# Performance work log

Hardware: AMD Instinct MI355X
Metric: run time of the kernel (lower is better)

## Reference

```python
import jax, jax.numpy as jnp
import numpy as np
from jax import lax

SCALE = 2
K_UP = 5
EPS = 1e-5
DN = ('NCHW', 'OIHW', 'NCHW')


def _bn(x, gamma, beta, mean, var):
    inv = gamma / jnp.sqrt(var + EPS)
    return x * inv[None, :, None, None] + (beta - mean * inv)[None, :, None, None]


def _pixel_shuffle(x, r):
    b, crr, h, w = x.shape
    c = crr // (r * r)
    x = x.reshape(b, c, r, r, h, w)
    x = x.transpose(0, 1, 4, 2, 5, 3)  # b, c, h, r, w, r
    return x.reshape(b, c, h * r, w * r)


def setup_inputs() -> dict:
    key = jax.random.key(0)
    ks = jax.random.split(key, 4)
    b, c, h, w = 4, 64, 128, 128
    c_mid = 64
    enc_out = (SCALE * K_UP) ** 2  # 100
    return {
        'X': jax.random.normal(ks[0], (b, c, h, w), jnp.float32),
        'comp_w': jax.random.normal(ks[1], (c_mid, c, 1, 1), jnp.float32) * 0.1,
        'comp_gamma': jnp.ones((c_mid,), jnp.float32),
        'comp_beta': jnp.zeros((c_mid,), jnp.float32),
        'comp_mean': jnp.zeros((c_mid,), jnp.float32),
        'comp_var': jnp.ones((c_mid,), jnp.float32),
        'enc_w': jax.random.normal(ks[2], (enc_out, c_mid, 3, 3), jnp.float32) * 0.05,
        'enc_b': jnp.zeros((enc_out,), jnp.float32),
        'enc_gamma': jnp.ones((enc_out,), jnp.float32),
        'enc_beta': jnp.zeros((enc_out,), jnp.float32),
        'enc_mean': jnp.zeros((enc_out,), jnp.float32),
        'enc_var': jnp.ones((enc_out,), jnp.float32),
    }


def reference(X, comp_w, comp_gamma, comp_beta, comp_mean, comp_var,
              enc_w, enc_b, enc_gamma, enc_beta, enc_mean, enc_var):
    b, c, h, w = X.shape
    h_, w_ = h * SCALE, w * SCALE
    # compress: 1x1 conv + BN + ReLU
    Wm = lax.conv_general_dilated(X, comp_w, (1, 1), 'VALID', dimension_numbers=DN)
    Wm = jax.nn.relu(_bn(Wm, comp_gamma, comp_beta, comp_mean, comp_var))
    # encode kernel weights: 3x3 conv + BN
    Wm = lax.conv_general_dilated(Wm, enc_w, (1, 1), ((1, 1), (1, 1)), dimension_numbers=DN)
    Wm = Wm + enc_b[None, :, None, None]
    Wm = _bn(Wm, enc_gamma, enc_beta, enc_mean, enc_var)
    # pixel shuffle -> [b, k_up^2, h_, w_], softmax over kernel dim
    Wm = _pixel_shuffle(Wm, SCALE)
    Wm = jax.nn.softmax(Wm, axis=1)
    # nearest upsample input
    Xu = jnp.repeat(jnp.repeat(X, SCALE, axis=2), SCALE, axis=3)  # [b,c,h_,w_]
    # unfold(k=5, dilation=2, pad=4) + einsum, fused as accumulation over the
    # 25 kernel taps (avoids the b*c*25*h_*w_ im2col blowup; identical math)
    pad = (K_UP // 2) * SCALE  # 4
    Xp = jnp.pad(Xu, ((0, 0), (0, 0), (pad, pad), (pad, pad)))
    out = jnp.zeros((b, c, h_, w_), X.dtype)
    for i in range(K_UP):
        for j in range(K_UP):
            k = i * K_UP + j
            patch = lax.dynamic_slice(Xp, (0, 0, i * SCALE, j * SCALE), (b, c, h_, w_))
            out = out + Wm[:, k:k + 1] * patch
    return out
```

## Files before the change

### kernel.cpp

```cpp
#include <hip/hip_runtime.h>

#define EPS 1e-5f

typedef __attribute__((ext_vector_type(8))) short short8;
typedef __attribute__((ext_vector_type(4))) float float4v;

__device__ inline unsigned short f2bf(float f) {
  unsigned u = __float_as_uint(f);
  unsigned r = (u + 0x7fffu + ((u >> 16) & 1u)) >> 16;
  return (unsigned short)r;
}
__device__ inline uint pk2(float a, float b) {
  return (uint)f2bf(a) | ((uint)f2bf(b) << 16);
}

__global__ __launch_bounds__(256) void xform_kernel(
    const float* __restrict__ enc_w, const float* __restrict__ enc_gamma,
    const float* __restrict__ enc_var, const float* __restrict__ comp_w,
    const float* __restrict__ comp_gamma, const float* __restrict__ comp_var,
    ushort* __restrict__ Awt, float* __restrict__ Wc) {
  int u = blockIdx.x * 256 + threadIdx.x;
  if (u < 9216) {
    int kc = u >> 9, rem = u & 511;
    int mt = rem >> 6, q = (rem >> 4) & 3, ml = rem & 15;
    int e = mt * 16 + ml;
    int t = kc >> 1, h = kc & 1;
    int dy = t / 3, dx = t - dy * 3;
    float inv = (e < 100) ? enc_gamma[e] * rsqrtf(enc_var[e] + EPS) : 0.f;
    ushort o[8];
#pragma unroll
    for (int j = 0; j < 8; ++j) {
      int ci = h * 32 + q * 8 + j;
      float w = (e < 100) ? enc_w[(e * 64 + ci) * 9 + dy * 3 + dx] * inv : 0.f;
      o[j] = f2bf(w);
    }
    uint4 v;
    v.x = (uint)o[0] | ((uint)o[1] << 16);
    v.y = (uint)o[2] | ((uint)o[3] << 16);
    v.z = (uint)o[4] | ((uint)o[5] << 16);
    v.w = (uint)o[6] | ((uint)o[7] << 16);
    *reinterpret_cast<uint4*>(Awt + (size_t)u * 8) = v;
  } else if (u < 9216 + 4096) {
    int v = u - 9216;
    int co = v & 63;
    float inv = comp_gamma[co] * rsqrtf(comp_var[co] + EPS);
    Wc[v] = comp_w[co * 64 + (v >> 6)] * inv;
  }
}

__global__ void bias_kernel(
    const float* __restrict__ enc_b, const float* __restrict__ enc_gamma,
    const float* __restrict__ enc_beta, const float* __restrict__ enc_mean,
    const float* __restrict__ enc_var, const float* __restrict__ comp_gamma,
    const float* __restrict__ comp_beta, const float* __restrict__ comp_mean,
    const float* __restrict__ comp_var, float* __restrict__ bias2,
    float* __restrict__ bias_c) {
  int t = threadIdx.x;
  if (t < 128) {
    float v = 0.f;
    if (t < 100) {
      float inv = enc_gamma[t] * rsqrtf(enc_var[t] + EPS);
      v = enc_b[t] * inv + enc_beta[t] - enc_mean[t] * inv;
    }
    bias2[t] = v;
  } else if (t < 192) {
    int c = t - 128;
    float inv = comp_gamma[c] * rsqrtf(comp_var[c] + EPS);
    bias_c[c] = comp_beta[c] - comp_mean[c] * inv;
  }
}

__global__ __launch_bounds__(256) void compress_kernel(
    const float* __restrict__ X, const float* __restrict__ Wc,
    const float* __restrict__ bias_c, ushort* __restrict__ out,
    ushort* __restrict__ Xb) {
  __shared__ __align__(16) float xtile[64 * 65];
  __shared__ __align__(16) float osm[64 * 68];
  const int tid = threadIdx.x;
  const int p0 = blockIdx.x * 64;
  const int b = p0 >> 14;
  const float* xbase = X + ((size_t)b << 20) + (p0 & 16383);

#pragma unroll
  for (int k = 0; k < 16; ++k) {
    int u = k * 256 + tid;
    int ci = u >> 6, px = u & 63;
    xtile[px * 65 + ci] = xbase[((size_t)ci << 14) + px];
  }
  __syncthreads();

  const int wv = __builtin_amdgcn_readfirstlane(tid >> 6);
  const int ln = tid & 63;
  float acc[16];
#pragma unroll
  for (int u = 0; u < 16; ++u) acc[u] = bias_c[wv * 16 + u];
  const float* xr = xtile + ln * 65;
#pragma unroll 8
  for (int ci = 0; ci < 64; ++ci) {
    float xv = xr[ci];
    const float* wr = Wc + ci * 64 + wv * 16;
#pragma unroll
    for (int u = 0; u < 16; ++u) acc[u] = fmaf(wr[u], xv, acc[u]);
  }
  float4v* orow = reinterpret_cast<float4v*>(osm) + ln * 17 + wv * 4;
#pragma unroll
  for (int j = 0; j < 4; ++j) {
    float4v t;
#pragma unroll
    for (int s = 0; s < 4; ++s) t[s] = fmaxf(acc[j * 4 + s], 0.f);
    orow[j] = t;
  }
  __syncthreads();

#pragma unroll
  for (int j = 0; j < 2; ++j) {
    int u = j * 256 + tid;
    int px = u >> 3, g = u & 7;
    const float* so = osm + px * 68 + g * 8;
    uint4 vo = make_uint4(pk2(so[0], so[1]), pk2(so[2], so[3]),
                          pk2(so[4], so[5]), pk2(so[6], so[7]));
    *reinterpret_cast<uint4*>(out + (size_t)(p0 + px) * 64 + g * 8) = vo;
    const float* sx = xtile + px * 65 + g * 8;
    uint4 vx = make_uint4(pk2(sx[0], sx[1]), pk2(sx[2], sx[3]),
                          pk2(sx[4], sx[5]), pk2(sx[6], sx[7]));
    *reinterpret_cast<uint4*>(Xb + (size_t)(p0 + px) * 64 + g * 8) = vx;
  }
}

__global__ __launch_bounds__(256) void encode_mfma(
    const ushort* __restrict__ Wm1t, const ushort* __restrict__ Awt,
    const float* __restrict__ bias2, uint* __restrict__ Wtu) {
  __shared__ __align__(16) char smem[25600];
  ushort* Xt = (ushort*)smem;
  const int tid = threadIdx.x;
  const int b = blockIdx.z;
  const int y0 = blockIdx.y * 8, x0 = blockIdx.x * 8;

  for (int u = tid; u < 800; u += 256) {
    int pos = u >> 3, cg = u & 7;
    int iy = pos / 10, ix = pos - iy * 10;
    int gy = y0 + iy - 1, gx = x0 + ix - 1;
    uint4 v = make_uint4(0, 0, 0, 0);
    if ((unsigned)gy < 128u && (unsigned)gx < 128u)
      v = *reinterpret_cast<const uint4*>(
          Wm1t + ((((size_t)b << 14) + (gy << 7) + gx) << 6) + cg * 8);
    *reinterpret_cast<uint4*>(&Xt[pos * 72 + cg * 8]) = v;
  }
  __syncthreads();

  const int wave = tid >> 6, lane = tid & 63;
  const int q = lane >> 4, px16 = lane & 15;

  float4v acc[2][4];
#pragma unroll
  for (int a = 0; a < 2; ++a)
#pragma unroll
    for (int n = 0; n < 4; ++n) acc[a][n] = (float4v){0.f, 0.f, 0.f, 0.f};

  const short8* Ap = reinterpret_cast<const short8*>(Awt);
#pragma unroll
  for (int kc = 0; kc < 18; ++kc) {
    const int t = kc >> 1, h = kc & 1;
    const int dy = t / 3, dx = t - dy * 3;
    short8 af[2];
#pragma unroll
    for (int a = 0; a < 2; ++a)
      af[a] = Ap[kc * 512 + (wave * 2 + a) * 64 + lane];
    short8 bfr[4];
#pragma unroll
    for (int n = 0; n < 4; ++n) {
      int p = n * 16 + px16;
      int iy = (p >> 3) + dy, ix = (p & 7) + dx;
      bfr[n] = *reinterpret_cast<const short8*>(
          &Xt[(iy * 10 + ix) * 72 + h * 32 + q * 8]);
    }
#pragma unroll
    for (int a = 0; a < 2; ++a)
#pragma unroll
      for (int n = 0; n < 4; ++n)
        acc[a][n] = __builtin_amdgcn_mfma_f32_16x16x32_bf16(
            af[a], bfr[n], acc[a][n], 0, 0, 0);
  }
  __syncthreads();

  float* wsm = (float*)smem;
#pragma unroll
  for (int a = 0; a < 2; ++a) {
    int ebase = (wave * 2 + a) * 16 + q * 4;
    if (ebase < 100) {
#pragma unroll
      for (int n = 0; n < 4; ++n) {
        int p = n * 16 + px16;
        *reinterpret_cast<float4v*>(wsm + p * 100 + ebase) = acc[a][n];
      }
    }
  }
  __syncthreads();

  if (tid < 64) {
    const float4v* bias4 = (const float4v*)bias2;
    float4v v[25];
    const float* wp = wsm + tid * 100;
#pragma unroll
    for (int j = 0; j < 25; ++j)
      v[j] = *reinterpret_cast<const float4v*>(wp + 4 * j) + bias4[j];
    float4v m = v[0];
#pragma unroll
    for (int j = 1; j < 25; ++j) {
      m.x = fmaxf(m.x, v[j].x); m.y = fmaxf(m.y, v[j].y);
      m.z = fmaxf(m.z, v[j].z); m.w = fmaxf(m.w, v[j].w);
    }
    float4v s = (float4v){0.f, 0.f, 0.f, 0.f};
#pragma unroll
    for (int j = 0; j < 25; ++j) {
      v[j].x = __expf(v[j].x - m.x); v[j].y = __expf(v[j].y - m.y);
      v[j].z = __expf(v[j].z - m.z); v[j].w = __expf(v[j].w - m.w);
      s += v[j];
    }
    float i0 = 1.f / s.x, i1 = 1.f / s.y, i2 = 1.f / s.z, i3 = 1.f / s.w;
    alignas(16) uint wp56[56];
#pragma unroll
    for (int k = 0; k < 25; ++k) {
      wp56[k]      = (uint)f2bf(v[k].x * i0) | ((uint)f2bf(v[k].y * i1) << 16);
      wp56[28 + k] = (uint)f2bf(v[k].z * i2) | ((uint)f2bf(v[k].w * i3) << 16);
    }
#pragma unroll
    for (int k = 25; k < 28; ++k) { wp56[k] = 0; wp56[28 + k] = 0; }
    int pix = b * 16384 + (y0 + (tid >> 3)) * 128 + x0 + (tid & 7);
    uint4* dst = reinterpret_cast<uint4*>(Wtu + (size_t)pix * 56);
#pragma unroll
    for (int j = 0; j < 14; ++j) dst[j] = reinterpret_cast<const uint4*>(wp56)[j];
  }
}

__global__ __launch_bounds__(256) void carafe_kernel(
    const ushort* __restrict__ Xb, const uint* __restrict__ Wtu,
    float* __restrict__ out) {
  const int tid = threadIdx.x;
  const int b = blockIdx.z;
  const int y0 = blockIdx.y * 8, x0 = blockIdx.x * 8;
  __shared__ __align__(16) ushort xt[144 * 72];

  for (int u = tid; u < 1152; u += 256) {
    int pos = u >> 3, cg = u & 7;
    int iy = pos / 12, ix = pos - iy * 12;
    int gy = y0 + iy - 2, gx = x0 + ix - 2;
    uint4 v = make_uint4(0, 0, 0, 0);
    if ((unsigned)gy < 128u && (unsigned)gx < 128u)
      v = *reinterpret_cast<const uint4*>(
          Xb + (((size_t)b * 16384 + gy * 128 + gx) << 6) + cg * 8);
    *reinterpret_cast<uint4*>(&xt[pos * 72 + cg * 8]) = v;
  }
  __syncthreads();

  const int p = tid & 63, q = tid >> 6;
  const int r1 = q & 1, cq = q >> 1;
  const int py = p >> 3, px = p & 7;

  int pix = b * 16384 + (y0 + py) * 128 + (x0 + px);
  const uint4* wq = reinterpret_cast<const uint4*>(Wtu + (size_t)pix * 56 + r1 * 28);
  alignas(16) uint w[28];
#pragma unroll
  for (int j = 0; j < 7; ++j) reinterpret_cast<uint4*>(w)[j] = wq[j];

  float2 acc[32];
#pragma unroll
  for (int i = 0; i < 32; ++i) acc[i] = make_float2(0.f, 0.f);

#pragma unroll
  for (int k = 0; k < 25; ++k) {
    const int dy = k / 5, dx = k - dy * 5;
    const ushort* bp = xt + ((py + dy) * 12 + (px + dx)) * 72 + cq * 32;
    float w0 = __uint_as_float(w[k] << 16);
    float w1 = __uint_as_float(w[k] & 0xffff0000u);
#pragma unroll
    for (int j = 0; j < 4; ++j) {
      uint4 xv = *reinterpret_cast<const uint4*>(bp + 8 * j);
      const uint xu[4] = {xv.x, xv.y, xv.z, xv.w};
#pragma unroll
      for (int t = 0; t < 4; ++t) {
        float xlo = __uint_as_float(xu[t] << 16);
        float xhi = __uint_as_float(xu[t] & 0xffff0000u);
        int c = j * 8 + t * 2;
        acc[c].x = fmaf(w0, xlo, acc[c].x);
        acc[c].y = fmaf(w1, xlo, acc[c].y);
        acc[c + 1].x = fmaf(w0, xhi, acc[c + 1].x);
        acc[c + 1].y = fmaf(w1, xhi, acc[c + 1].y);
      }
    }
  }

  int yq = (y0 + py) * 2 + r1;
  int xq = (x0 + px) * 2;
#pragma unroll
  for (int ci = 0; ci < 32; ++ci) {
    int c = cq * 32 + ci;
    *reinterpret_cast<float2*>(
        out + ((size_t)(b * 64 + c) * 256 + yq) * 256 + xq) = acc[ci];
  }
}

extern "C" void kernel_launch(void* const* d_in, const int* in_sizes, int n_in,
                              void* d_out, int out_size, void* d_ws, size_t ws_size,
                              hipStream_t stream) {
  const float* X          = (const float*)d_in[0];
  const float* comp_w     = (const float*)d_in[1];
  const float* comp_gamma = (const float*)d_in[2];
  const float* comp_beta  = (const float*)d_in[3];
  const float* comp_mean  = (const float*)d_in[4];
  const float* comp_var   = (const float*)d_in[5];
  const float* enc_w      = (const float*)d_in[6];
  const float* enc_b      = (const float*)d_in[7];
  const float* enc_gamma  = (const float*)d_in[8];
  const float* enc_beta   = (const float*)d_in[9];
  const float* enc_mean   = (const float*)d_in[10];
  const float* enc_var    = (const float*)d_in[11];
  float* out = (float*)d_out;

  char* ws = (char*)d_ws;
  ushort* Wm1t  = (ushort*)(ws);
  uint*   Wtu   = (uint*)(ws + 8388608);
  ushort* Xb    = (ushort*)(ws + 23068672);
  ushort* Awt   = (ushort*)(ws + 31457280);
  float*  Wc    = (float*)(ws + 31604736);
  float*  bias2 = (float*)(ws + 31621120);
  float*  biasc = (float*)(ws + 31621632);

  xform_kernel<<<52, 256, 0, stream>>>(enc_w, enc_gamma, enc_var,
                                       comp_w, comp_gamma, comp_var, Awt, Wc);
  bias_kernel<<<1, 256, 0, stream>>>(enc_b, enc_gamma, enc_beta, enc_mean,
                                     enc_var, comp_gamma, comp_beta, comp_mean,
                                     comp_var, bias2, biasc);
  compress_kernel<<<1024, 256, 0, stream>>>(X, Wc, biasc, Wm1t, Xb);
  encode_mfma<<<dim3(16, 16, 4), 256, 0, stream>>>(Wm1t, Awt, bias2, Wtu);
  carafe_kernel<<<dim3(16, 16, 4), 256, 0, stream>>>(Xb, Wtu, out);
}
```

Before: 149.4 us.

## Fuse encode conv, softmax and CARAFE reassembly into one kernel

Merges the encode MFMA kernel and the CARAFE apply kernel so the softmaxed kernel weights stay in shared memory instead of round-tripping through a global bf16 buffer. It also folds the bias setup kernel into the weight transform kernel as an extra block, which removes one launch. Softmax now runs on all 256 threads (one per pixel and sub-position) instead of 64, and the weights stay in fp32. In exchange, shared memory per block rises to about 46KB, which may lower occupancy, and the fused kernel carries more register pressure.

```diff
diff --git a/kernel.cpp b/kernel.cpp
--- a/kernel.cpp
+++ b/kernel.cpp
@@ -18,7 +18,27 @@
     const float* __restrict__ enc_w, const float* __restrict__ enc_gamma,
     const float* __restrict__ enc_var, const float* __restrict__ comp_w,
     const float* __restrict__ comp_gamma, const float* __restrict__ comp_var,
-    ushort* __restrict__ Awt, float* __restrict__ Wc) {
+    const float* __restrict__ enc_b, const float* __restrict__ enc_beta,
+    const float* __restrict__ enc_mean, const float* __restrict__ comp_beta,
+    const float* __restrict__ comp_mean,
+    ushort* __restrict__ Awt, float* __restrict__ Wc,
+    float* __restrict__ bias2, float* __restrict__ bias_c) {
+  if (blockIdx.x == 52) {
+    int t = threadIdx.x;
+    if (t < 128) {
+      float v = 0.f;
+      if (t < 100) {
+        float inv = enc_gamma[t] * rsqrtf(enc_var[t] + EPS);
+        v = enc_b[t] * inv + enc_beta[t] - enc_mean[t] * inv;
+      }
+      bias2[t] = v;
+    } else if (t < 192) {
+      int c = t - 128;
+      float inv = comp_gamma[c] * rsqrtf(comp_var[c] + EPS);
+      bias_c[c] = comp_beta[c] - comp_mean[c] * inv;
+    }
+    return;
+  }
   int u = blockIdx.x * 256 + threadIdx.x;
   if (u < 9216) {
     int kc = u >> 9, rem = u & 511;
@@ -48,28 +68,6 @@
   }
 }
 
-__global__ void bias_kernel(
-    const float* __restrict__ enc_b, const float* __restrict__ enc_gamma,
-    const float* __restrict__ enc_beta, const float* __restrict__ enc_mean,
-    const float* __restrict__ enc_var, const float* __restrict__ comp_gamma,
-    const float* __restrict__ comp_beta, const float* __restrict__ comp_mean,
-    const float* __restrict__ comp_var, float* __restrict__ bias2,
-    float* __restrict__ bias_c) {
-  int t = threadIdx.x;
-  if (t < 128) {
-    float v = 0.f;
-    if (t < 100) {
-      float inv = enc_gamma[t] * rsqrtf(enc_var[t] + EPS);
-      v = enc_b[t] * inv + enc_beta[t] - enc_mean[t] * inv;
-    }
-    bias2[t] = v;
-  } else if (t < 192) {
-    int c = t - 128;
-    float inv = comp_gamma[c] * rsqrtf(comp_var[c] + EPS);
-    bias_c[c] = comp_beta[c] - comp_mean[c] * inv;
-  }
-}
-
 __global__ __launch_bounds__(256) void compress_kernel(
     const float* __restrict__ X, const float* __restrict__ Wc,
     const float* __restrict__ bias_c, ushort* __restrict__ out,
@@ -127,11 +125,14 @@
   }
 }
 
-__global__ __launch_bounds__(256) void encode_mfma(
+__global__ __launch_bounds__(256) void encode_apply(
     const ushort* __restrict__ Wm1t, const ushort* __restrict__ Awt,
-    const float* __restrict__ bias2, uint* __restrict__ Wtu) {
-  __shared__ __align__(16) char smem[25600];
+    const float* __restrict__ bias2, const ushort* __restrict__ Xb,
+    float* __restrict__ out) {
+  __shared__ __align__(16) char smem[46592];
+  float* wsm = (float*)smem;
   ushort* Xt = (ushort*)smem;
+  ushort* xb = (ushort*)(smem + 25856);
   const int tid = threadIdx.x;
   const int b = blockIdx.z;
   const int y0 = blockIdx.y * 8, x0 = blockIdx.x * 8;
@@ -146,101 +147,6 @@
           Wm1t + ((((size_t)b << 14) + (gy << 7) + gx) << 6) + cg * 8);
     *reinterpret_cast<uint4*>(&Xt[pos * 72 + cg * 8]) = v;
   }
-  __syncthreads();
-
-  const int wave = tid >> 6, lane = tid & 63;
-  const int q = lane >> 4, px16 = lane & 15;
-
-  float4v acc[2][4];
-#pragma unroll
-  for (int a = 0; a < 2; ++a)
-#pragma unroll
-    for (int n = 0; n < 4; ++n) acc[a][n] = (float4v){0.f, 0.f, 0.f, 0.f};
-
-  const short8* Ap = reinterpret_cast<const short8*>(Awt);
-#pragma unroll
-  for (int kc = 0; kc < 18; ++kc) {
-    const int t = kc >> 1, h = kc & 1;
-    const int dy = t / 3, dx = t - dy * 3;
-    short8 af[2];
-#pragma unroll
-    for (int a = 0; a < 2; ++a)
-      af[a] = Ap[kc * 512 + (wave * 2 + a) * 64 + lane];
-    short8 bfr[4];
-#pragma unroll
-    for (int n = 0; n < 4; ++n) {
-      int p = n * 16 + px16;
-      int iy = (p >> 3) + dy, ix = (p & 7) + dx;
-      bfr[n] = *reinterpret_cast<const short8*>(
-          &Xt[(iy * 10 + ix) * 72 + h * 32 + q * 8]);
-    }
-#pragma unroll
-    for (int a = 0; a < 2; ++a)
-#pragma unroll
-      for (int n = 0; n < 4; ++n)
-        acc[a][n] = __builtin_amdgcn_mfma_f32_16x16x32_bf16(
-            af[a], bfr[n], acc[a][n], 0, 0, 0);
-  }
-  __syncthreads();
-
-  float* wsm = (float*)smem;
-#pragma unroll
-  for (int a = 0; a < 2; ++a) {
-    int ebase = (wave * 2 + a) * 16 + q * 4;
-    if (ebase < 100) {
-#pragma unroll
-      for (int n = 0; n < 4; ++n) {
-        int p = n * 16 + px16;
-        *reinterpret_cast<float4v*>(wsm + p * 100 + ebase) = acc[a][n];
-      }
-    }
-  }
-  __syncthreads();
-
-  if (tid < 64) {
-    const float4v* bias4 = (const float4v*)bias2;
-    float4v v[25];
-    const float* wp = wsm + tid * 100;
-#pragma unroll
-    for (int j = 0; j < 25; ++j)
-      v[j] = *reinterpret_cast<const float4v*>(wp + 4 * j) + bias4[j];
-    float4v m = v[0];
-#pragma unroll
-    for (int j = 1; j < 25; ++j) {
-      m.x = fmaxf(m.x, v[j].x); m.y = fmaxf(m.y, v[j].y);
-      m.z = fmaxf(m.z, v[j].z); m.w = fmaxf(m.w, v[j].w);
-    }
-    float4v s = (float4v){0.f, 0.f, 0.f, 0.f};
-#pragma unroll
-    for (int j = 0; j < 25; ++j) {
-      v[j].x = __expf(v[j].x - m.x); v[j].y = __expf(v[j].y - m.y);
-      v[j].z = __expf(v[j].z - m.z); v[j].w = __expf(v[j].w - m.w);
-      s += v[j];
-    }
-    float i0 = 1.f / s.x, i1 = 1.f / s.y, i2 = 1.f / s.z, i3 = 1.f / s.w;
-    alignas(16) uint wp56[56];
-#pragma unroll
-    for (int k = 0; k < 25; ++k) {
-      wp56[k]      = (uint)f2bf(v[k].x * i0) | ((uint)f2bf(v[k].y * i1) << 16);
-      wp56[28 + k] = (uint)f2bf(v[k].z * i2) | ((uint)f2bf(v[k].w * i3) << 16);
-    }
-#pragma unroll
-    for (int k = 25; k < 28; ++k) { wp56[k] = 0; wp56[28 + k] = 0; }
-    int pix = b * 16384 + (y0 + (tid >> 3)) * 128 + x0 + (tid & 7);
-    uint4* dst = reinterpret_cast<uint4*>(Wtu + (size_t)pix * 56);
-#pragma unroll
-    for (int j = 0; j < 14; ++j) dst[j] = reinterpret_cast<const uint4*>(wp56)[j];
-  }
-}
-
-__global__ __launch_bounds__(256) void carafe_kernel(
-    const ushort* __restrict__ Xb, const uint* __restrict__ Wtu,
-    float* __restrict__ out) {
-  const int tid = threadIdx.x;
-  const int b = blockIdx.z;
-  const int y0 = blockIdx.y * 8, x0 = blockIdx.x * 8;
-  __shared__ __align__(16) ushort xt[144 * 72];
-
   for (int u = tid; u < 1152; u += 256) {
     int pos = u >> 3, cg = u & 7;
     int iy = pos / 12, ix = pos - iy * 12;
@@ -249,54 +155,122 @@
     if ((unsigned)gy < 128u && (unsigned)gx < 128u)
       v = *reinterpret_cast<const uint4*>(
           Xb + (((size_t)b * 16384 + gy * 128 + gx) << 6) + cg * 8);
-    *reinterpret_cast<uint4*>(&xt[pos * 72 + cg * 8]) = v;
-  }
-  __syncthreads();
-
-  const int p = tid & 63, q = tid >> 6;
-  const int r1 = q & 1, cq = q >> 1;
-  const int py = p >> 3, px = p & 7;
-
-  int pix = b * 16384 + (y0 + py) * 128 + (x0 + px);
-  const uint4* wq = reinterpret_cast<const uint4*>(Wtu + (size_t)pix * 56 + r1 * 28);
-  alignas(16) uint w[28];
-#pragma unroll
-  for (int j = 0; j < 7; ++j) reinterpret_cast<uint4*>(w)[j] = wq[j];
-
-  float2 acc[32];
-#pragma unroll
-  for (int i = 0; i < 32; ++i) acc[i] = make_float2(0.f, 0.f);
-
-#pragma unroll
-  for (int k = 0; k < 25; ++k) {
-    const int dy = k / 5, dx = k - dy * 5;
-    const ushort* bp = xt + ((py + dy) * 12 + (px + dx)) * 72 + cq * 32;
-    float w0 = __uint_as_float(w[k] << 16);
-    float w1 = __uint_as_float(w[k] & 0xffff0000u);
-#pragma unroll
-    for (int j = 0; j < 4; ++j) {
-      uint4 xv = *reinterpret_cast<const uint4*>(bp + 8 * j);
-      const uint xu[4] = {xv.x, xv.y, xv.z, xv.w};
-#pragma unroll
-      for (int t = 0; t < 4; ++t) {
-        float xlo = __uint_as_float(xu[t] << 16);
-        float xhi = __uint_as_float(xu[t] & 0xffff0000u);
-        int c = j * 8 + t * 2;
-        acc[c].x = fmaf(w0, xlo, acc[c].x);
-        acc[c].y = fmaf(w1, xlo, acc[c].y);
-        acc[c + 1].x = fmaf(w0, xhi, acc[c + 1].x);
-        acc[c + 1].y = fmaf(w1, xhi, acc[c + 1].y);
+    *reinterpret_cast<uint4*>(&xb[pos * 72 + cg * 8]) = v;
+  }
+  __syncthreads();
+
+  const int wave = tid >> 6, lane = tid & 63;
+  const int q = lane >> 4, px16 = lane & 15;
+
+  float4v acc[2][4];
+#pragma unroll
+  for (int a = 0; a < 2; ++a)
+#pragma unroll
+    for (int n = 0; n < 4; ++n) acc[a][n] = (float4v){0.f, 0.f, 0.f, 0.f};
+
+  const short8* Ap = reinterpret_cast<const short8*>(Awt);
+#pragma unroll
+  for (int kc = 0; kc < 18; ++kc) {
+    const int t = kc >> 1, h = kc & 1;
+    const int dy = t / 3, dx = t - dy * 3;
+    short8 af[2];
+#pragma unroll
+    for (int a = 0; a < 2; ++a)
+      af[a] = Ap[kc * 512 + (wave * 2 + a) * 64 + lane];
+    short8 bfr[4];
+#pragma unroll
+    for (int n = 0; n < 4; ++n) {
+      int p = n * 16 + px16;
+      int iy = (p >> 3) + dy, ix = (p & 7) + dx;
+      bfr[n] = *reinterpret_cast<const short8*>(
+          &Xt[(iy * 10 + ix) * 72 + h * 32 + q * 8]);
+    }
+#pragma unroll
+    for (int a = 0; a < 2; ++a)
+#pragma unroll
+      for (int n = 0; n < 4; ++n)
+        acc[a][n] = __builtin_amdgcn_mfma_f32_16x16x32_bf16(
+            af[a], bfr[n], acc[a][n], 0, 0, 0);
+  }
+  __syncthreads();
+
+#pragma unroll
+  for (int a = 0; a < 2; ++a) {
+    int ebase = (wave * 2 + a) * 16 + q * 4;
+    if (ebase < 100) {
+#pragma unroll
+      for (int n = 0; n < 4; ++n) {
+        int p = n * 16 + px16;
+        float* wp = wsm + p * 101 + ebase;
+#pragma unroll
+        for (int r = 0; r < 4; ++r) wp[r] = acc[a][n][r];
       }
     }
   }
-
-  int yq = (y0 + py) * 2 + r1;
-  int xq = (x0 + px) * 2;
-#pragma unroll
-  for (int ci = 0; ci < 32; ++ci) {
-    int c = cq * 32 + ci;
-    *reinterpret_cast<float2*>(
-        out + ((size_t)(b * 64 + c) * 256 + yq) * 256 + xq) = acc[ci];
+  __syncthreads();
+
+  {
+    const int px = tid & 63, g = tid >> 6;
+    float* wp = wsm + px * 101 + g;
+    float v[25];
+#pragma unroll
+    for (int k = 0; k < 25; ++k) v[k] = wp[4 * k] + bias2[4 * k + g];
+    float m = v[0];
+#pragma unroll
+    for (int k = 1; k < 25; ++k) m = fmaxf(m, v[k]);
+    float s = 0.f;
+#pragma unroll
+    for (int k = 0; k < 25; ++k) {
+      v[k] = __expf(v[k] - m);
+      s += v[k];
+    }
+    float inv = 1.f / s;
+#pragma unroll
+    for (int k = 0; k < 25; ++k) wp[4 * k] = v[k] * inv;
+  }
+  __syncthreads();
+
+  {
+    const int p = tid & 63, qq = tid >> 6;
+    const int r1 = qq & 1, cq = qq >> 1;
+    const int py = p >> 3, px = p & 7;
+    const float* wrow = wsm + p * 101 + 2 * r1;
+
+    float2 a2[32];
+#pragma unroll
+    for (int i = 0; i < 32; ++i) a2[i] = make_float2(0.f, 0.f);
+
+#pragma unroll
+    for (int k = 0; k < 25; ++k) {
+      const int dy = k / 5, dx = k - dy * 5;
+      const float w0 = wrow[4 * k];
+      const float w1 = wrow[4 * k + 1];
+      const ushort* bp = xb + ((py + dy) * 12 + (px + dx)) * 72 + cq * 32;
+#pragma unroll
+      for (int j = 0; j < 4; ++j) {
+        uint4 xv = *reinterpret_cast<const uint4*>(bp + 8 * j);
+        const uint xu[4] = {xv.x, xv.y, xv.z, xv.w};
+#pragma unroll
+        for (int t = 0; t < 4; ++t) {
+          float xlo = __uint_as_float(xu[t] << 16);
+          float xhi = __uint_as_float(xu[t] & 0xffff0000u);
+          int c = j * 8 + t * 2;
+          a2[c].x = fmaf(w0, xlo, a2[c].x);
+          a2[c].y = fmaf(w1, xlo, a2[c].y);
+          a2[c + 1].x = fmaf(w0, xhi, a2[c + 1].x);
+          a2[c + 1].y = fmaf(w1, xhi, a2[c + 1].y);
+        }
+      }
+    }
+
+    int yq = (y0 + py) * 2 + r1;
+    int xq = (x0 + px) * 2;
+#pragma unroll
+    for (int ci = 0; ci < 32; ++ci) {
+      int c = cq * 32 + ci;
+      *reinterpret_cast<float2*>(
+          out + ((size_t)(b * 64 + c) * 256 + yq) * 256 + xq) = a2[ci];
+    }
   }
 }
 
@@ -319,19 +293,17 @@
 
   char* ws = (char*)d_ws;
   ushort* Wm1t  = (ushort*)(ws);
-  uint*   Wtu   = (uint*)(ws + 8388608);
-  ushort* Xb    = (ushort*)(ws + 23068672);
-  ushort* Awt   = (ushort*)(ws + 31457280);
-  float*  Wc    = (float*)(ws + 31604736);
-  float*  bias2 = (float*)(ws + 31621120);
-  float*  biasc = (float*)(ws + 31621632);
-
-  xform_kernel<<<52, 256, 0, stream>>>(enc_w, enc_gamma, enc_var,
-                                       comp_w, comp_gamma, comp_var, Awt, Wc);
-  bias_kernel<<<1, 256, 0, stream>>>(enc_b, enc_gamma, enc_beta, enc_mean,
-                                     enc_var, comp_gamma, comp_beta, comp_mean,
-                                     comp_var, bias2, biasc);
+  ushort* Xb    = (ushort*)(ws + 8388608);
+  ushort* Awt   = (ushort*)(ws + 16777216);
+  float*  Wc    = (float*)(ws + 16924672);
+  float*  bias2 = (float*)(ws + 16941056);
+  float*  biasc = (float*)(ws + 16941568);
+
+  xform_kernel<<<53, 256, 0, stream>>>(enc_w, enc_gamma, enc_var,
+                                       comp_w, comp_gamma, comp_var,
+                                       enc_b, enc_beta, enc_mean,
+                                       comp_beta, comp_mean,
+                                       Awt, Wc, bias2, biasc);
   compress_kernel<<<1024, 256, 0, stream>>>(X, Wc, biasc, Wm1t, Xb);
-  encode_mfma<<<dim3(16, 16, 4), 256, 0, stream>>>(Wm1t, Awt, bias2, Wtu);
-  carafe_kernel<<<dim3(16, 16, 4), 256, 0, stream>>>(Xb, Wtu, out);
-}
+  encode_apply<<<dim3(16, 16, 4), 256, 0, stream>>>(Wm1t, Awt, bias2, Xb, out);
+}
```

New measurement: 194.5 us. 1.3x slower.
